# Optimization experiments

Measured on AMD Instinct MI355X. Metric: run time of the kernel, lower is better.

The kernel has to match this reference:

```python
import jax, jax.numpy as jnp
import numpy as np

NUM_CLASSES = 2   # module init num_classes; class logits have NUM_CLASSES+1 (incl. 'no object')
ORIG_H, ORIG_W = 512, 512  # original input resolution that masks are upsampled to


def setup_inputs() -> dict:
    key = jax.random.key(0)
    k1, k2 = jax.random.split(key)
    B, Q = 8, 100
    h, w = 128, 128  # mask decoder outputs at 1/4 input resolution
    class_queries_logits = jax.random.normal(k1, (B, Q, NUM_CLASSES + 1), dtype=jnp.float32)
    masks_queries_logits = jax.random.normal(k2, (B, Q, h, w), dtype=jnp.float32)
    return {"class_queries_logits": class_queries_logits,
            "masks_queries_logits": masks_queries_logits}


def reference(class_queries_logits, masks_queries_logits):
    B, Q = masks_queries_logits.shape[:2]
    # bilinear upsample to original resolution (align_corners=False == half-pixel centers)
    masks_up = jax.image.resize(masks_queries_logits, (B, Q, ORIG_H, ORIG_W), method="bilinear")
    # softmax over classes (incl. no-object), keep only the first NUM_CLASSES,
    # exactly as the original loop only indexes c in range(num_classes)
    class_probs = jax.nn.softmax(class_queries_logits, axis=-1)[..., :NUM_CLASSES]  # [B,Q,C]
    mask_probs = jax.nn.sigmoid(masks_up)  # [B,Q,H,W]
    # fused replacement for the triple b/q/c Python loop of weighted accumulates
    logits = jnp.einsum("bqc,bqhw->bchw", class_probs, mask_probs)  # [B,C,H,W]
    return logits
```

## Files before the change

### kernel.cpp

```cpp
#include <hip/hip_runtime.h>
#include <math.h>

#define NB 8
#define NQ 100
#define NQH 50
#define NCP1 3
#define NC 2
#define HIN 128
#define WIN 128
#define HOUT 512
#define WOUT 512
#define QSTR (HIN * WIN)
#define QBYTES (QSTR * 4)

#if __has_builtin(__builtin_amdgcn_exp2f)
#define EXP2F(x) __builtin_amdgcn_exp2f(x)
#else
#define EXP2F(x) exp2f(x)
#endif
#if __has_builtin(__builtin_amdgcn_rcpf)
#define RCPF(x) __builtin_amdgcn_rcpf(x)
#else
#define RCPF(x) (1.0f / (x))
#endif

__device__ __forceinline__ float bperm(int byteaddr, float v) {
  return __int_as_float(__builtin_amdgcn_ds_bpermute(byteaddr, __float_as_int(v)));
}

typedef unsigned int u32x4 __attribute__((ext_vector_type(4)));

__global__ __launch_bounds__(512, 4)
void m2f_fused(const float* __restrict__ cls,
               const float* __restrict__ masks,
               float* __restrict__ out) {
  const int b   = blockIdx.x;
  const int k   = blockIdx.y;
  const int tid = threadIdx.x;

  __shared__ float  sigtab[4096];
  __shared__ float2 pq[NQ];
  __shared__ float  part[8][256];

#pragma unroll
  for (int j = 0; j < 8; ++j) {
    const int i = tid + j * 512;
    const float x = (float)i * 0.0078125f - 16.0f;
    sigtab[i] = RCPF(1.0f + EXP2F(x));
  }

  if (tid < NQ) {
    const float* cl = cls + (b * NQ + tid) * NCP1;
    float a0 = cl[0], a1 = cl[1], a2 = cl[2];
    float mx = fmaxf(a0, fmaxf(a1, a2));
    const float L2E = 1.4426950408889634f;
    float e0 = EXP2F((a0 - mx) * L2E);
    float e1 = EXP2F((a1 - mx) * L2E);
    float e2 = EXP2F((a2 - mx) * L2E);
    float inv = RCPF(e0 + e1 + e2);
    pq[tid] = make_float2(e0 * inv, e1 * inv);
  }
  __syncthreads();

  const int wave = tid >> 6;
  const int r    = wave & 3;
  const int qh   = wave >> 2;
  const int lane = tid & 63;
  const int q0   = qh * NQH;

  const int rlo = (r < 2) ? (k > 0 ? k - 1 : 0) : k;
  const int rhi = (r < 2) ? k : (k < HIN - 1 ? k + 1 : HIN - 1);
  const float NL2E128 = -1.4426950408889634f * 128.0f;
  const float wlo = ((r == 0) ? 0.375f : (r == 1) ? 0.125f
                   : (r == 2) ? 0.875f : 0.625f) * NL2E128;
  const float whi = ((r == 0) ? 0.625f : (r == 1) ? 0.875f
                   : (r == 2) ? 0.125f : 0.375f) * NL2E128;

  union { const float* p; unsigned long long u; } pn;
  pn.p = masks + (size_t)b * NQ * QSTR;
  u32x4 srd;
  srd.x = (unsigned int)pn.u;
  srd.y = (unsigned int)(pn.u >> 32) & 0xFFFFu;
  srd.z = (unsigned int)(NQ * QSTR * 4);
  srd.w = 0x00020000u;

  const int voffA = q0 * QBYTES + (rlo * WIN + 2 * lane) * 4;
  const int voffB = q0 * QBYTES + (rhi * WIN + 2 * lane) * 4;

  const int addrL = (lane - 1) << 2;
  const int addrR = (lane + 1) << 2;
  const bool edgeL = (lane == 0);
  const bool edgeR = (lane == 63);

  float2 aSL = make_float2(0.f, 0.f);
  float2 aS0 = make_float2(0.f, 0.f);
  float2 aSM = make_float2(0.f, 0.f);
  float2 aS1 = make_float2(0.f, 0.f);

  float2 A0, B0, A1, B1, A2, B2, A3, B3, A4, B4, A5, B5, A6, B6, A7, B7;
  float sP0, sP1, sP2, sP3, sC0, sC1, sC2, sC3;

#define LOADSET(S, qrel)                                                  \
  do {                                                                    \
    asm volatile("buffer_load_dwordx2 %0, %2, %3, 0 offen\n\t"            \
                 "buffer_load_dwordx2 %1, %4, %3, 0 offen"                \
                 : "=&v"(A##S), "=&v"(B##S)                               \
                 : "v"(voffA + (qrel) * QBYTES), "s"(srd),                \
                   "v"(voffB + (qrel) * QBYTES));                         \
  } while (0)

#define WT(S, N)                                                          \
  asm volatile("s_waitcnt vmcnt(" #N ")" : "+v"(A##S), "+v"(B##S))

#define SIG(u, sout)                                                      \
  do {                                                                    \
    float uc = fminf(fmaxf((u), 0.0f), 4095.0f);                          \
    sout = sigtab[(int)uc];                                               \
  } while (0)

#define GATHER(S)                                                         \
  do {                                                                    \
    float u0 = fmaf(wlo, A##S.x, fmaf(whi, B##S.x, 2048.5f));             \
    float u1 = fmaf(wlo, A##S.y, fmaf(whi, B##S.y, 2048.5f));             \
    float uLr = bperm(addrL, u1);                                         \
    float um = 0.5f * (u0 + u1);                                          \
    SIG(u0, sC1);                                                         \
    SIG(um, sC2);                                                         \
    SIG(u1, sC3);                                                         \
    float uL = edgeL ? u0 : uLr;                                          \
    float umL = 0.5f * (uL + u0);                                         \
    SIG(umL, sC0);                                                        \
  } while (0)

#define ACCROLL(qqprev)                                                   \
  do {                                                                    \
    const float2 pd = pq[qqprev];                                         \
    aSL.x = fmaf(pd.x, sP0, aSL.x);  aSL.y = fmaf(pd.y, sP0, aSL.y);      \
    aS0.x = fmaf(pd.x, sP1, aS0.x);  aS0.y = fmaf(pd.y, sP1, aS0.y);      \
    aSM.x = fmaf(pd.x, sP2, aSM.x);  aSM.y = fmaf(pd.y, sP2, aSM.y);      \
    aS1.x = fmaf(pd.x, sP3, aS1.x);  aS1.y = fmaf(pd.y, sP3, aS1.y);      \
    sP0 = sC0; sP1 = sC1; sP2 = sC2; sP3 = sC3;                           \
  } while (0)

#define PH(S, s)                                                          \
  do {                                                                    \
    WT(S, 14);                                                            \
    GATHER(S);                                                            \
    LOADSET(S, (s) + 8);                                                  \
    ACCROLL(q0 + (s) - 1);                                                \
  } while (0)

  LOADSET(0, 0); LOADSET(1, 1); LOADSET(2, 2); LOADSET(3, 3);
  LOADSET(4, 4); LOADSET(5, 5); LOADSET(6, 6); LOADSET(7, 7);

  WT(0, 14);
  GATHER(0);
  sP0 = sC0; sP1 = sC1; sP2 = sC2; sP3 = sC3;
  LOADSET(0, 8);

  for (int q = 1; q < 41; q += 8) {
    PH(1, q);     PH(2, q + 1); PH(3, q + 2); PH(4, q + 3);
    PH(5, q + 4); PH(6, q + 5); PH(7, q + 6); PH(0, q + 7);
  }
  PH(1, 41);

  WT(2, 14); GATHER(2); ACCROLL(q0 + 41);
  WT(3, 12); GATHER(3); ACCROLL(q0 + 42);
  WT(4, 10); GATHER(4); ACCROLL(q0 + 43);
  WT(5, 8);  GATHER(5); ACCROLL(q0 + 44);
  WT(6, 6);  GATHER(6); ACCROLL(q0 + 45);
  WT(7, 4);  GATHER(7); ACCROLL(q0 + 46);
  WT(0, 2);  GATHER(0); ACCROLL(q0 + 47);
  WT(1, 0);  GATHER(1); ACCROLL(q0 + 48);
  {
    const float2 pd = pq[q0 + 49];
    aSL.x = fmaf(pd.x, sP0, aSL.x);  aSL.y = fmaf(pd.y, sP0, aSL.y);
    aS0.x = fmaf(pd.x, sP1, aS0.x);  aS0.y = fmaf(pd.y, sP1, aS0.y);
    aSM.x = fmaf(pd.x, sP2, aSM.x);  aSM.y = fmaf(pd.y, sP2, aSM.y);
    aS1.x = fmaf(pd.x, sP3, aS1.x);  aS1.y = fmaf(pd.y, sP3, aS1.y);
  }

  const int col = r * 64 + lane;
  if (qh == 1) {
    part[0][col] = aSL.x;  part[1][col] = aSL.y;
    part[2][col] = aS0.x;  part[3][col] = aS0.y;
    part[4][col] = aSM.x;  part[5][col] = aSM.y;
    part[6][col] = aS1.x;  part[7][col] = aS1.y;
  }
  __syncthreads();
  if (qh == 0) {
    aSL.x += part[0][col];  aSL.y += part[1][col];
    aS0.x += part[2][col];  aS0.y += part[3][col];
    aSM.x += part[4][col];  aSM.y += part[5][col];
    aS1.x += part[6][col];  aS1.y += part[7][col];

    float SRx_r = bperm(addrR, aSL.x);
    float SRy_r = bperm(addrR, aSL.y);
    float SRx = edgeR ? aS1.x : SRx_r;
    float SRy = edgeR ? aS1.y : SRy_r;

    float o0x = fmaf(0.25f, aS0.x, 0.75f * aSL.x);
    float o1x = fmaf(0.75f, aS0.x, 0.25f * aSL.x);
    float o2x = fmaf(0.25f, aSM.x, 0.75f * aS0.x);
    float o3x = fmaf(0.75f, aSM.x, 0.25f * aS0.x);
    float o4x = fmaf(0.25f, aS1.x, 0.75f * aSM.x);
    float o5x = fmaf(0.75f, aS1.x, 0.25f * aSM.x);
    float o6x = fmaf(0.25f, SRx,   0.75f * aS1.x);
    float o7x = fmaf(0.75f, SRx,   0.25f * aS1.x);
    float o0y = fmaf(0.25f, aS0.y, 0.75f * aSL.y);
    float o1y = fmaf(0.75f, aS0.y, 0.25f * aSL.y);
    float o2y = fmaf(0.25f, aSM.y, 0.75f * aS0.y);
    float o3y = fmaf(0.75f, aSM.y, 0.25f * aS0.y);
    float o4y = fmaf(0.25f, aS1.y, 0.75f * aSM.y);
    float o5y = fmaf(0.75f, aS1.y, 0.25f * aSM.y);
    float o6y = fmaf(0.25f, SRy,   0.75f * aS1.y);
    float o7y = fmaf(0.75f, SRy,   0.25f * aS1.y);

    const int y  = 4 * k + r;
    const int x0 = 8 * lane;
    float* o0 = out + (((size_t)b * NC + 0) * HOUT + y) * WOUT + x0;
    float* o1 = out + (((size_t)b * NC + 1) * HOUT + y) * WOUT + x0;
    *(float4*)o0       = make_float4(o0x, o1x, o2x, o3x);
    *(float4*)(o0 + 4) = make_float4(o4x, o5x, o6x, o7x);
    *(float4*)o1       = make_float4(o0y, o1y, o2y, o3y);
    *(float4*)(o1 + 4) = make_float4(o4y, o5y, o6y, o7y);
  }
}

extern "C" void kernel_launch(void* const* d_in, const int* in_sizes, int n_in,
                              void* d_out, int out_size, void* d_ws, size_t ws_size,
                              hipStream_t stream) {
  const float* cls   = (const float*)d_in[0];
  const float* masks = (const float*)d_in[1];
  float* out = (float*)d_out;
  dim3 grid(NB, HIN);
  m2f_fused<<<grid, 512, 0, stream>>>(cls, masks, out);
}
```

Baseline: 113.4 us.

## Software-pipeline LDS sigmoid-table lookups across queries with explicit lgkmcnt waits

Replaces the compiler-scheduled sigmoid table gathers and bpermute with inline-asm ds_read/ds_bpermute issued one query ahead, alternating even/odd register sets. Manual lgkmcnt waits plus sched_barrier keep LDS latency overlapped with the FMA accumulation of the previous query. This raises register use and depends on exact LDS counter bookkeeping in asm; a wrong count would break correctness.

```diff
diff --git a/kernel.cpp b/kernel.cpp
--- a/kernel.cpp
+++ b/kernel.cpp
@@ -68,6 +68,9 @@
   const int lane = tid & 63;
   const int q0   = qh * NQH;
 
+  const unsigned tabb = (unsigned)(size_t)&sigtab[0];
+  const unsigned pqb  = (unsigned)(size_t)&pq[0];
+
   const int rlo = (r < 2) ? (k > 0 ? k - 1 : 0) : k;
   const int rhi = (r < 2) ? k : (k < HIN - 1 ? k + 1 : HIN - 1);
   const float NL2E128 = -1.4426950408889634f * 128.0f;
@@ -98,7 +101,9 @@
   float2 aS1 = make_float2(0.f, 0.f);
 
   float2 A0, B0, A1, B1, A2, B2, A3, B3, A4, B4, A5, B5, A6, B6, A7, B7;
-  float sP0, sP1, sP2, sP3, sC0, sC1, sC2, sC3;
+  float  u0E, u1E, uLrE, sgE0, sgE1, sgE2, sgE3;
+  float  u0O, u1O, uLrO, sgO0, sgO1, sgO2, sgO3;
+  float2 pdE, pdO;
 
 #define LOADSET(S, qrel)                                                  \
   do {                                                                    \
@@ -112,73 +117,123 @@
 #define WT(S, N)                                                          \
   asm volatile("s_waitcnt vmcnt(" #N ")" : "+v"(A##S), "+v"(B##S))
 
-#define SIG(u, sout)                                                      \
-  do {                                                                    \
-    float uc = fminf(fmaxf((u), 0.0f), 4095.0f);                          \
-    sout = sigtab[(int)uc];                                               \
-  } while (0)
-
-#define GATHER(S)                                                         \
-  do {                                                                    \
-    float u0 = fmaf(wlo, A##S.x, fmaf(whi, B##S.x, 2048.5f));             \
-    float u1 = fmaf(wlo, A##S.y, fmaf(whi, B##S.y, 2048.5f));             \
-    float uLr = bperm(addrL, u1);                                         \
-    float um = 0.5f * (u0 + u1);                                          \
-    SIG(u0, sC1);                                                         \
-    SIG(um, sC2);                                                         \
-    SIG(u1, sC3);                                                         \
-    float uL = edgeL ? u0 : uLr;                                          \
-    float umL = 0.5f * (uL + u0);                                         \
-    SIG(umL, sC0);                                                        \
-  } while (0)
-
-#define ACCROLL(qqprev)                                                   \
-  do {                                                                    \
-    const float2 pd = pq[qqprev];                                         \
-    aSL.x = fmaf(pd.x, sP0, aSL.x);  aSL.y = fmaf(pd.y, sP0, aSL.y);      \
-    aS0.x = fmaf(pd.x, sP1, aS0.x);  aS0.y = fmaf(pd.y, sP1, aS0.y);      \
-    aSM.x = fmaf(pd.x, sP2, aSM.x);  aSM.y = fmaf(pd.y, sP2, aSM.y);      \
-    aS1.x = fmaf(pd.x, sP3, aS1.x);  aS1.y = fmaf(pd.y, sP3, aS1.y);      \
-    sP0 = sC0; sP1 = sC1; sP2 = sC2; sP3 = sC3;                           \
-  } while (0)
-
-#define PH(S, s)                                                          \
-  do {                                                                    \
-    WT(S, 14);                                                            \
-    GATHER(S);                                                            \
-    LOADSET(S, (s) + 8);                                                  \
-    ACCROLL(q0 + (s) - 1);                                                \
+#define DSR32(dst, addr)                                                  \
+  asm volatile("ds_read_b32 %0, %1" : "=v"(dst) : "v"(addr))
+#define DSR64(dst, addr)                                                  \
+  asm volatile("ds_read_b64 %0, %1" : "=v"(dst) : "v"(addr))
+#define BPERMA(dst, src)                                                  \
+  asm volatile("ds_bpermute_b32 %0, %1, %2"                               \
+               : "=v"(dst) : "v"(addrL), "v"(src))
+
+#define SIGA(u)                                                           \
+  (tabb + (((unsigned)(int)fminf(fmaxf((u), 0.0f), 4095.0f)) << 2))
+
+#define LGKMW6(C, X)                                                      \
+  do {                                                                    \
+    asm volatile("s_waitcnt lgkmcnt(2)"                                   \
+                 : "+v"(uLr##C), "+v"(pd##X), "+v"(sg##X##0),             \
+                   "+v"(sg##X##1), "+v"(sg##X##2), "+v"(sg##X##3));       \
+    __builtin_amdgcn_sched_barrier(0);                                    \
+  } while (0)
+
+#define ACC(X)                                                            \
+  do {                                                                    \
+    aSL.x = fmaf(pd##X.x, sg##X##0, aSL.x);                               \
+    aSL.y = fmaf(pd##X.y, sg##X##0, aSL.y);                               \
+    aS0.x = fmaf(pd##X.x, sg##X##1, aS0.x);                               \
+    aS0.y = fmaf(pd##X.y, sg##X##1, aS0.y);                               \
+    aSM.x = fmaf(pd##X.x, sg##X##2, aSM.x);                               \
+    aSM.y = fmaf(pd##X.y, sg##X##2, aSM.y);                               \
+    aS1.x = fmaf(pd##X.x, sg##X##3, aS1.x);                               \
+    aS1.y = fmaf(pd##X.y, sg##X##3, aS1.y);                               \
+  } while (0)
+
+#define MIDG(C)                                                           \
+  do {                                                                    \
+    float uL  = edgeL ? u0##C : uLr##C;                                   \
+    float um  = 0.5f * (u0##C + u1##C);                                   \
+    float umL = 0.5f * (uL + u0##C);                                      \
+    DSR32(sg##C##0, SIGA(umL));                                           \
+    DSR32(sg##C##1, SIGA(u0##C));                                         \
+    DSR32(sg##C##2, SIGA(um));                                            \
+    DSR32(sg##C##3, SIGA(u1##C));                                         \
+  } while (0)
+
+#define BODY(ST, C, X, s)                                                 \
+  do {                                                                    \
+    WT(ST, 14);                                                           \
+    u0##X = fmaf(wlo, A##ST.x, fmaf(whi, B##ST.x, 2048.5f));              \
+    u1##X = fmaf(wlo, A##ST.y, fmaf(whi, B##ST.y, 2048.5f));              \
+    BPERMA(uLr##X, u1##X);                                                \
+    DSR64(pd##C, pqb + (unsigned)((q0 + (s)) * 8));                       \
+    LGKMW6(C, X);                                                         \
+    MIDG(C);                                                              \
+    ACC(X);                                                               \
+    LOADSET(ST, (s) + 9);                                                 \
+  } while (0)
+
+#define BODYNL(ST, VM, C, X, s)                                           \
+  do {                                                                    \
+    WT(ST, VM);                                                           \
+    u0##X = fmaf(wlo, A##ST.x, fmaf(whi, B##ST.x, 2048.5f));              \
+    u1##X = fmaf(wlo, A##ST.y, fmaf(whi, B##ST.y, 2048.5f));              \
+    BPERMA(uLr##X, u1##X);                                                \
+    DSR64(pd##C, pqb + (unsigned)((q0 + (s)) * 8));                       \
+    LGKMW6(C, X);                                                         \
+    MIDG(C);                                                              \
+    ACC(X);                                                               \
   } while (0)
 
   LOADSET(0, 0); LOADSET(1, 1); LOADSET(2, 2); LOADSET(3, 3);
   LOADSET(4, 4); LOADSET(5, 5); LOADSET(6, 6); LOADSET(7, 7);
 
   WT(0, 14);
-  GATHER(0);
-  sP0 = sC0; sP1 = sC1; sP2 = sC2; sP3 = sC3;
+  u0E = fmaf(wlo, A0.x, fmaf(whi, B0.x, 2048.5f));
+  u1E = fmaf(wlo, A0.y, fmaf(whi, B0.y, 2048.5f));
+  BPERMA(uLrE, u1E);
   LOADSET(0, 8);
 
+  WT(1, 14);
+  u0O = fmaf(wlo, A1.x, fmaf(whi, B1.x, 2048.5f));
+  u1O = fmaf(wlo, A1.y, fmaf(whi, B1.y, 2048.5f));
+  BPERMA(uLrO, u1O);
+  DSR64(pdE, pqb + (unsigned)((q0 + 0) * 8));
+  asm volatile("s_waitcnt lgkmcnt(2)" : "+v"(uLrE));
+  __builtin_amdgcn_sched_barrier(0);
+  MIDG(E);
+  LOADSET(1, 9);
+
   for (int q = 1; q < 41; q += 8) {
-    PH(1, q);     PH(2, q + 1); PH(3, q + 2); PH(4, q + 3);
-    PH(5, q + 4); PH(6, q + 5); PH(7, q + 6); PH(0, q + 7);
-  }
-  PH(1, 41);
-
-  WT(2, 14); GATHER(2); ACCROLL(q0 + 41);
-  WT(3, 12); GATHER(3); ACCROLL(q0 + 42);
-  WT(4, 10); GATHER(4); ACCROLL(q0 + 43);
-  WT(5, 8);  GATHER(5); ACCROLL(q0 + 44);
-  WT(6, 6);  GATHER(6); ACCROLL(q0 + 45);
-  WT(7, 4);  GATHER(7); ACCROLL(q0 + 46);
-  WT(0, 2);  GATHER(0); ACCROLL(q0 + 47);
-  WT(1, 0);  GATHER(1); ACCROLL(q0 + 48);
-  {
-    const float2 pd = pq[q0 + 49];
-    aSL.x = fmaf(pd.x, sP0, aSL.x);  aSL.y = fmaf(pd.y, sP0, aSL.y);
-    aS0.x = fmaf(pd.x, sP1, aS0.x);  aS0.y = fmaf(pd.y, sP1, aS0.y);
-    aSM.x = fmaf(pd.x, sP2, aSM.x);  aSM.y = fmaf(pd.y, sP2, aSM.y);
-    aS1.x = fmaf(pd.x, sP3, aS1.x);  aS1.y = fmaf(pd.y, sP3, aS1.y);
-  }
+    BODY(2, O, E, q);
+    BODY(3, E, O, q + 1);
+    BODY(4, O, E, q + 2);
+    BODY(5, E, O, q + 3);
+    BODY(6, O, E, q + 4);
+    BODY(7, E, O, q + 5);
+    BODY(0, O, E, q + 6);
+    BODY(1, E, O, q + 7);
+  }
+
+  BODYNL(2, 14, O, E, 41);
+  BODYNL(3, 12, E, O, 42);
+  BODYNL(4, 10, O, E, 43);
+  BODYNL(5, 8,  E, O, 44);
+  BODYNL(6, 6,  O, E, 45);
+  BODYNL(7, 4,  E, O, 46);
+  BODYNL(0, 2,  O, E, 47);
+  BODYNL(1, 0,  E, O, 48);
+
+  DSR64(pdO, pqb + (unsigned)((q0 + 49) * 8));
+  asm volatile("s_waitcnt lgkmcnt(1)"
+               : "+v"(uLrO), "+v"(pdE), "+v"(sgE0), "+v"(sgE1),
+                 "+v"(sgE2), "+v"(sgE3));
+  __builtin_amdgcn_sched_barrier(0);
+  MIDG(O);
+  ACC(E);
+  asm volatile("s_waitcnt lgkmcnt(0)"
+               : "+v"(pdO), "+v"(sgO0), "+v"(sgO1), "+v"(sgO2), "+v"(sgO3));
+  __builtin_amdgcn_sched_barrier(0);
+  ACC(O);
 
   const int col = r * 64 + lane;
   if (qh == 1) {
```

Measured after the change: 120.7 us. 1.06x slower.
